# Optimization experiments

Measured on AMD Instinct MI355X. Metric: run time of the kernel, lower is better.

Reference implementation:

```python
import jax, jax.numpy as jnp
import numpy as np

DIM = 768
HEADS = 12
HEAD_DIM = DIM // HEADS
SCALE = HEAD_DIM ** -0.5


def setup_inputs() -> dict:
    key = jax.random.key(0)
    k1, k2, k3, k4, k5 = jax.random.split(key, 5)
    B, N = 4, 2048
    x = jax.random.normal(k1, (B, N, DIM), dtype=jnp.float32)
    # qkv Linear: weight [3*dim, dim], bias [3*dim]
    w_qkv = jax.random.normal(k2, (3 * DIM, DIM), dtype=jnp.float32) * (DIM ** -0.5)
    b_qkv = jax.random.normal(k3, (3 * DIM,), dtype=jnp.float32) * 0.01
    # proj Linear: weight [dim, dim], bias [dim]
    w_proj = jax.random.normal(k4, (DIM, DIM), dtype=jnp.float32) * (DIM ** -0.5)
    b_proj = jax.random.normal(k5, (DIM,), dtype=jnp.float32) * 0.01
    return {"x": x, "w_qkv": w_qkv, "b_qkv": b_qkv, "w_proj": w_proj, "b_proj": b_proj}


def reference(x, w_qkv, b_qkv, w_proj, b_proj):
    B, N, C = x.shape
    qkv = (jnp.einsum('bnc,oc->bno', x, w_qkv) + b_qkv)
    qkv = qkv.reshape(B, N, 3, HEADS, HEAD_DIM).transpose(2, 0, 3, 1, 4)
    q, k, v = qkv[0], qkv[1], qkv[2]
    attn = jnp.einsum('bhqd,bhkd->bhqk', q, k) * SCALE
    attn = jax.nn.softmax(attn, axis=-1)
    out = jnp.einsum('bhqk,bhkd->bhqd', attn, v)  # [B, H, N, Dh]
    out = out.transpose(0, 2, 1, 3).reshape(B, N, C)
    # dropout is identity in eval mode
    return jnp.einsum('bnc,oc->bno', out, w_proj) + b_proj
```

## Files before the change

kernel.cpp:

```cpp
#include <hip/hip_runtime.h>
#include <hip/hip_bf16.h>

using bf16 = __hip_bfloat16;
typedef __bf16 bf16x8 __attribute__((ext_vector_type(8)));
typedef short short4v __attribute__((ext_vector_type(4)));
typedef short short8v __attribute__((ext_vector_type(8)));
typedef float float4v __attribute__((ext_vector_type(4)));

#define DIM   768
#define NH    12
#define HD    64
#define SEQ   2048
#define BATCH 4
#define TOK   (BATCH * SEQ)
#define SCALE_QL2E 0.18033688011112042f

#define NX  (TOK * DIM)
#define NWQ (3 * DIM * DIM)
#define NWP (DIM * DIM)

__device__ __forceinline__ short f2bf(float f) {
  union { bf16 h; short s; } u;
  u.h = __float2bfloat16(f);
  return u.s;
}

union frag8 { short4v h[2]; short8v s; bf16x8 b; };

__device__ __forceinline__ void async_copy16(const bf16* g, short* l) {
  __builtin_amdgcn_global_load_lds(
      (const __attribute__((address_space(1))) unsigned int*)g,
      (__attribute__((address_space(3))) unsigned int*)l, 16, 0, 0);
}

__global__ void __launch_bounds__(256)
cvt3(const float* __restrict__ a, bf16* __restrict__ oa, long na,
     const float* __restrict__ b, bf16* __restrict__ ob, long nb,
     const float* __restrict__ c, bf16* __restrict__ oc, long nc) {
  const long i = ((long)blockIdx.x * 256 + threadIdx.x) * 8;
  const float* src; bf16* dst; long off;
  if (i < na)                { src = a; dst = oa; off = i; }
  else if (i < na + nb)      { src = b; dst = ob; off = i - na; }
  else if (i < na + nb + nc) { src = c; dst = oc; off = i - na - nb; }
  else return;
  const float4v x0 = *(const float4v*)(src + off);
  const float4v x1 = *(const float4v*)(src + off + 4);
  short8v r;
  r[0] = f2bf(x0[0]); r[1] = f2bf(x0[1]); r[2] = f2bf(x0[2]); r[3] = f2bf(x0[3]);
  r[4] = f2bf(x1[0]); r[5] = f2bf(x1[1]); r[6] = f2bf(x1[2]); r[7] = f2bf(x1[3]);
  *(short8v*)(dst + off) = r;
}

__device__ __forceinline__ void gemm_mainloop(const bf16* __restrict__ A,
                                              const bf16* __restrict__ B,
                                              short* As, short* Bs,
                                              float4v acc[4][4]) {
  const int t = threadIdx.x;
  const int w = t >> 6, l = t & 63, lr = l & 15, q = l >> 4;
  const int wr = ((w >> 1) << 6), wc = ((w & 1) << 6);

  const bf16* Ag = A + (t >> 2) * DIM + (t & 3) * 8;
  const bf16* Bg = B + (t >> 2) * DIM + (t & 3) * 8;

  for (int k0 = 0; k0 < DIM; k0 += 32) {
    __syncthreads();
    async_copy16(Ag,            &As[t * 8]);
    async_copy16(Ag + 64 * DIM, &As[2048 + t * 8]);
    async_copy16(Bg,            &Bs[t * 8]);
    async_copy16(Bg + 64 * DIM, &Bs[2048 + t * 8]);
    Ag += 32; Bg += 32;
    __syncthreads();

    bf16x8 af[4], bfv[4];
#pragma unroll
    for (int i = 0; i < 4; ++i)
      af[i] = *(const bf16x8*)&As[(wr + i * 16 + lr) * 32 + q * 8];
#pragma unroll
    for (int j = 0; j < 4; ++j)
      bfv[j] = *(const bf16x8*)&Bs[(wc + j * 16 + lr) * 32 + q * 8];
#pragma unroll
    for (int i = 0; i < 4; ++i)
#pragma unroll
      for (int j = 0; j < 4; ++j)
        acc[i][j] = __builtin_amdgcn_mfma_f32_16x16x32_bf16(af[i], bfv[j],
                                                            acc[i][j], 0, 0, 0);
  }
}

__global__ void __launch_bounds__(256)
gemm_qkv(const bf16* __restrict__ X, const bf16* __restrict__ W,
         const float* __restrict__ bias,
         bf16* __restrict__ qb, bf16* __restrict__ kb, bf16* __restrict__ vb) {
  __shared__ short As[128 * 32];
  __shared__ short Bs[128 * 32];
  const int t = threadIdx.x;
  const int w = t >> 6, l = t & 63, lr = l & 15, q = l >> 4;
  const int wr = ((w >> 1) << 6), wc = ((w & 1) << 6);
  const int row0 = blockIdx.y * 128, col0 = blockIdx.x * 128;

  float4v acc[4][4] = {};
  gemm_mainloop(X + row0 * DIM, W + col0 * DIM, As, Bs, acc);

#pragma unroll
  for (int j = 0; j < 4; ++j) {
    const int gn = col0 + wc + j * 16 + lr;
    const int which = gn / DIM;
    const int cc = gn - which * DIM;
    const int hh = cc >> 6, dd = cc & 63;
    const float bv = bias[gn];
#pragma unroll
    for (int i = 0; i < 4; ++i) {
      const int gm0 = row0 + wr + i * 16 + (q << 2);
      const int b = gm0 >> 11, n0 = gm0 & 2047;
      if (which == 2) {
        short4v pv;
#pragma unroll
        for (int r = 0; r < 4; ++r) pv[r] = f2bf(acc[i][j][r] + bv);
        *(short4v*)&vb[((size_t)(b * NH + hh) * HD + dd) * SEQ + n0] = pv;
      } else {
        bf16* dst = (which == 0) ? qb : kb;
        const float sc = (which == 0) ? SCALE_QL2E : 1.0f;
#pragma unroll
        for (int r = 0; r < 4; ++r)
          dst[((size_t)(b * NH + hh) * SEQ + n0 + r) * HD + dd] =
              __float2bfloat16((acc[i][j][r] + bv) * sc);
      }
    }
  }
}

__global__ void __launch_bounds__(256, 3)
flash_attn(const bf16* __restrict__ Qp, const bf16* __restrict__ Kp,
           const bf16* __restrict__ Vtp, bf16* __restrict__ Op) {
  const int bh = blockIdx.y, qt = blockIdx.x;
  const int t = threadIdx.x, w = t >> 6, l = t & 63, lr = l & 15, q = l >> 4;
  __shared__ short Ks[128 * 72];
  __shared__ short Vt[64 * 136];

  const bf16* Qb = Qp  + (size_t)(bh * SEQ + qt * 128) * HD;
  const bf16* Kb = Kp  + (size_t)bh * SEQ * HD;
  const bf16* Vb = Vtp + (size_t)bh * HD * SEQ;

  const int tr3 = t >> 3, td8 = (t & 7) * 8;
  const int tr4 = t >> 4, tc8 = (t & 15) * 8;

  short8v kr[4], vr[4];
#pragma unroll
  for (int i = 0; i < 4; ++i) {
    kr[i] = *(const short8v*)(Kb + (size_t)(i * 32 + tr3) * HD + td8);
    vr[i] = *(const short8v*)(Vb + (size_t)(i * 16 + tr4) * SEQ + tc8);
  }

#pragma unroll
  for (int i = 0; i < 4; ++i)
    *(short8v*)&Ks[(i * 32 + tr3) * 72 + td8] =
        *(const short8v*)(Qb + (size_t)(i * 32 + tr3) * HD + td8);
  __syncthreads();
  bf16x8 qf[2][2];
#pragma unroll
  for (int it = 0; it < 2; ++it)
#pragma unroll
    for (int kq = 0; kq < 2; ++kq)
      qf[it][kq] = *(const bf16x8*)&Ks[(w * 32 + it * 16 + lr) * 72 + kq * 32 + q * 8];

  float4v o[2][4] = {};
  float l_run[2] = {0.f, 0.f};

  for (int kt = 0; kt < 16; ++kt) {
    __syncthreads();
#pragma unroll
    for (int i = 0; i < 4; ++i) {
      *(short8v*)&Ks[(i * 32 + tr3) * 72 + td8]  = kr[i];
      *(short8v*)&Vt[(i * 16 + tr4) * 136 + tc8] = vr[i];
    }
    __syncthreads();
    if (kt < 15) {
      const int k1 = (kt + 1) * 128;
#pragma unroll
      for (int i = 0; i < 4; ++i) {
        kr[i] = *(const short8v*)(Kb + (size_t)(k1 + i * 32 + tr3) * HD + td8);
        vr[i] = *(const short8v*)(Vb + (size_t)(i * 16 + tr4) * SEQ + k1 + tc8);
      }
    }

    float4v s[8][2] = {};
#pragma unroll
    for (int jn = 0; jn < 8; ++jn) {
      bf16x8 kf[2];
#pragma unroll
      for (int kq = 0; kq < 2; ++kq)
        kf[kq] = *(const bf16x8*)&Ks[(jn * 16 + lr) * 72 + kq * 32 + q * 8];
#pragma unroll
      for (int it = 0; it < 2; ++it)
#pragma unroll
        for (int kq = 0; kq < 2; ++kq)
          s[jn][it] = __builtin_amdgcn_mfma_f32_16x16x32_bf16(kf[kq], qf[it][kq],
                                                              s[jn][it], 0, 0, 0);
    }

    frag8 pf[4][2];
#pragma unroll
    for (int it = 0; it < 2; ++it) {
      float ls = 0.f;
#pragma unroll
      for (int jn = 0; jn < 8; ++jn)
#pragma unroll
        for (int r = 0; r < 4; ++r) {
          const float p = __builtin_amdgcn_exp2f(s[jn][it][r]);
          s[jn][it][r] = p;
          ls += p;
        }
      l_run[it] += ls;
#pragma unroll
      for (int c4 = 0; c4 < 4; ++c4) {
#pragma unroll
        for (int r = 0; r < 4; ++r) {
          pf[c4][it].s[r]     = f2bf(s[2 * c4][it][r]);
          pf[c4][it].s[4 + r] = f2bf(s[2 * c4 + 1][it][r]);
        }
      }
    }

#pragma unroll
    for (int c4 = 0; c4 < 4; ++c4) {
#pragma unroll
      for (int dj = 0; dj < 4; ++dj) {
        frag8 vf;
        vf.h[0] = *(const short4v*)&Vt[(dj * 16 + lr) * 136 + c4 * 32 + (q << 2)];
        vf.h[1] = *(const short4v*)&Vt[(dj * 16 + lr) * 136 + c4 * 32 + 16 + (q << 2)];
#pragma unroll
        for (int it = 0; it < 2; ++it)
          o[it][dj] = __builtin_amdgcn_mfma_f32_16x16x32_bf16(pf[c4][it].b, vf.b,
                                                              o[it][dj], 0, 0, 0);
      }
    }
  }

  const int b = bh / NH, h = bh - b * NH;
#pragma unroll
  for (int it = 0; it < 2; ++it) {
    l_run[it] += __shfl_xor(l_run[it], 16);
    l_run[it] += __shfl_xor(l_run[it], 32);
    const float li = 1.0f / l_run[it];
#pragma unroll
    for (int r = 0; r < 4; ++r) {
      const float linv = __shfl(li, (q << 2) + r, 64);
      const int grow = b * SEQ + qt * 128 + w * 32 + it * 16 + (q << 2) + r;
      bf16* orow = Op + (size_t)grow * DIM + h * HD;
#pragma unroll
      for (int dj = 0; dj < 4; ++dj)
        orow[dj * 16 + lr] = __float2bfloat16(o[it][dj][r] * linv);
    }
  }
}

__global__ void __launch_bounds__(256)
gemm_proj(const bf16* __restrict__ A, const bf16* __restrict__ W,
          const float* __restrict__ bias, float* __restrict__ out) {
  __shared__ short As[128 * 32];
  __shared__ short Bs[128 * 32];
  const int t = threadIdx.x;
  const int w = t >> 6, l = t & 63, lr = l & 15, q = l >> 4;
  const int wr = ((w >> 1) << 6), wc = ((w & 1) << 6);
  const int row0 = blockIdx.y * 128, col0 = blockIdx.x * 128;

  float4v acc[4][4] = {};
  gemm_mainloop(A + row0 * DIM, W + col0 * DIM, As, Bs, acc);

#pragma unroll
  for (int j = 0; j < 4; ++j) {
    const int gn = col0 + wc + j * 16 + lr;
    const float bv = bias[gn];
#pragma unroll
    for (int i = 0; i < 4; ++i) {
#pragma unroll
      for (int r = 0; r < 4; ++r) {
        const int gm = row0 + wr + i * 16 + (q << 2) + r;
        out[(size_t)gm * DIM + gn] = acc[i][j][r] + bv;
      }
    }
  }
}

extern "C" void kernel_launch(void* const* d_in, const int* in_sizes, int n_in,
                              void* d_out, int out_size, void* d_ws, size_t ws_size,
                              hipStream_t stream) {
  const float* x      = (const float*)d_in[0];
  const float* w_qkv  = (const float*)d_in[1];
  const float* b_qkv  = (const float*)d_in[2];
  const float* w_proj = (const float*)d_in[3];
  const float* b_proj = (const float*)d_in[4];
  float* out = (float*)d_out;

  const size_t perbuf = (size_t)BATCH * NH * SEQ * HD;
  bf16* qb  = (bf16*)d_ws;
  bf16* kb  = qb + perbuf;
  bf16* vb  = kb + perbuf;
  bf16* ao  = vb + perbuf;
  bf16* xb  = ao + perbuf;
  bf16* wqb = xb + (size_t)NX;
  bf16* wpb = wqb + (size_t)NWQ;

  const int cvt_blocks = (NX + NWQ + NWP) / 8 / 256;
  cvt3<<<cvt_blocks, 256, 0, stream>>>(x, xb, NX, w_qkv, wqb, NWQ, w_proj, wpb, NWP);
  gemm_qkv <<<dim3(3 * DIM / 128, TOK / 128), 256, 0, stream>>>(xb, wqb, b_qkv, qb, kb, vb);
  flash_attn<<<dim3(SEQ / 128, BATCH * NH),   256, 0, stream>>>(qb, kb, vb, ao);
  gemm_proj <<<dim3(DIM / 128, TOK / 128),    256, 0, stream>>>(ao, wpb, b_proj, out);
}
```

Baseline: 211.9 us.

## Rewrite QKV GEMM as 256x256-tile, 512-thread async double-buffered pipeline

Replaces the 128x128 QKV GEMM with a 256x256 tile kernel using 8 waves. It uses async global-to-LDS copies with double buffering, XOR swizzled LDS layout and interleaved barriers with MFMA priority boosts. It also adds a block-index swizzle for L2 locality. The aim is to hide global load latency and raise MFMA utilisation. The cost is more LDS (128KB) and register pressure, and a fixed launch of 288 blocks that assumes these exact sizes.

Measured after the change: 213.1 us. About the same (+0.6%).

```diff
diff --git a/kernel.cpp b/kernel.cpp
--- a/kernel.cpp
+++ b/kernel.cpp
@@ -87,35 +87,122 @@
   }
 }
 
-__global__ void __launch_bounds__(256)
+#define STG(gp, c, slot, k0)                                                  \
+  async_copy16((gp) + (k0),      &lds[c][slot][t * 8]);                       \
+  async_copy16((gp) + (k0) + 32, &lds[c][slot][4096 + t * 8])
+
+#define RD_A(dst, C, slot)                                                    \
+  _Pragma("unroll") for (int f_ = 0; f_ < 4; ++f_) {                          \
+    dst[f_][0] = *(const bf16x8*)&lds[C][slot][f_ * 1024 + arow32 + acol];    \
+    dst[f_][1] = *(const bf16x8*)&lds[C][slot][4096 + f_ * 1024 + arow32 + acol]; \
+  }
+
+#define RD_B(dst, C, slot)                                                    \
+  _Pragma("unroll") for (int g_ = 0; g_ < 2; ++g_) {                          \
+    dst[g_][0] = *(const bf16x8*)&lds[C][slot][g_ * 2048 + brow32 + acol];    \
+    dst[g_][1] = *(const bf16x8*)&lds[C][slot][4096 + g_ * 2048 + brow32 + acol]; \
+  }
+
+#define MFMA8(AF, BF, MO, NO)                                                 \
+  _Pragma("unroll") for (int f_ = 0; f_ < 4; ++f_)                            \
+  _Pragma("unroll") for (int g_ = 0; g_ < 2; ++g_) {                          \
+    acc[(MO) + f_][(NO) + g_] = __builtin_amdgcn_mfma_f32_16x16x32_bf16(      \
+        AF[f_][0], BF[g_][0], acc[(MO) + f_][(NO) + g_], 0, 0, 0);            \
+    acc[(MO) + f_][(NO) + g_] = __builtin_amdgcn_mfma_f32_16x16x32_bf16(      \
+        AF[f_][1], BF[g_][1], acc[(MO) + f_][(NO) + g_], 0, 0, 0);            \
+  }
+
+#define BARRIER __builtin_amdgcn_s_barrier()
+#define LGKM0 asm volatile("s_waitcnt lgkmcnt(0)" ::: "memory")
+#define VW6 asm volatile("s_waitcnt vmcnt(6)" ::: "memory")
+#define VW0 asm volatile("s_waitcnt vmcnt(0)" ::: "memory")
+#define NOSTG (void)0
+
+#define KTILE(C, ST1, ST2, ST3, ST4, VW)                                      \
+  {                                                                           \
+    bf16x8 a0[4][2], a1[4][2], b0[2][2], b1[2][2];                            \
+    RD_A(a0, C, 0); RD_B(b0, C, 2);                                           \
+    ST1; BARRIER; LGKM0;                                                      \
+    __builtin_amdgcn_s_setprio(1); MFMA8(a0, b0, 0, 0);                       \
+    __builtin_amdgcn_s_setprio(0); BARRIER;                                   \
+    RD_B(b1, C, 3);                                                           \
+    ST2; BARRIER; LGKM0;                                                      \
+    __builtin_amdgcn_s_setprio(1); MFMA8(a0, b1, 0, 2);                       \
+    __builtin_amdgcn_s_setprio(0); BARRIER;                                   \
+    RD_A(a1, C, 1);                                                           \
+    ST3; BARRIER; LGKM0;                                                      \
+    __builtin_amdgcn_s_setprio(1); MFMA8(a1, b0, 4, 0);                       \
+    __builtin_amdgcn_s_setprio(0); BARRIER;                                   \
+    ST4; BARRIER;                                                             \
+    __builtin_amdgcn_s_setprio(1); MFMA8(a1, b1, 4, 2);                       \
+    __builtin_amdgcn_s_setprio(0); VW; BARRIER;                               \
+  }
+
+__global__ void __launch_bounds__(512, 2)
 gemm_qkv(const bf16* __restrict__ X, const bf16* __restrict__ W,
          const float* __restrict__ bias,
          bf16* __restrict__ qb, bf16* __restrict__ kb, bf16* __restrict__ vb) {
-  __shared__ short As[128 * 32];
-  __shared__ short Bs[128 * 32];
+  __shared__ short lds[2][4][8192];
   const int t = threadIdx.x;
   const int w = t >> 6, l = t & 63, lr = l & 15, q = l >> 4;
-  const int wr = ((w >> 1) << 6), wc = ((w & 1) << 6);
-  const int row0 = blockIdx.y * 128, col0 = blockIdx.x * 128;
-
-  float4v acc[4][4] = {};
-  gemm_mainloop(X + row0 * DIM, W + col0 * DIM, As, Bs, acc);
-
-#pragma unroll
-  for (int j = 0; j < 4; ++j) {
-    const int gn = col0 + wc + j * 16 + lr;
+  const int wm = w >> 2, wn = w & 3;
+
+  const int orig = blockIdx.x;
+  const int swz = (orig & 7) * 36 + (orig >> 3);
+  const int tm = swz / 9, tn = swz - tm * 9;
+  const int row0 = tm * 256, col0 = tn * 256;
+
+  const int sr = t >> 2;
+  const int sswz = (((sr >> 3) & 1) << 4) | (((sr >> 1) & 1) << 3);
+  const int scol = (((t & 3) << 3) ^ sswz);
+  const bf16* pa0 = X + (size_t)(row0 +       sr) * DIM + scol;
+  const bf16* pa1 = X + (size_t)(row0 + 128 + sr) * DIM + scol;
+  const bf16* pb0 = W + (size_t)(col0 +       sr) * DIM + scol;
+  const bf16* pb1 = W + (size_t)(col0 + 128 + sr) * DIM + scol;
+
+  const int rswz = (((lr >> 3) & 1) << 4) | (((lr >> 1) & 1) << 3);
+  const int acol = ((q << 3) ^ rswz);
+  const int arow32 = (wm * 16 + lr) * 32;
+  const int brow32 = (wn * 16 + lr) * 32;
+
+  float4v acc[8][4] = {};
+
+  STG(pa0, 0, 0, 0);
+  STG(pb0, 0, 2, 0);
+  STG(pb1, 0, 3, 0);
+  STG(pa1, 0, 1, 0);
+  STG(pa0, 1, 0, 64);
+  STG(pb0, 1, 2, 64);
+  STG(pb1, 1, 3, 64);
+  asm volatile("s_waitcnt vmcnt(6)" ::: "memory");
+  BARRIER;
+
+#pragma unroll 1
+  for (int i = 0; i < 5; ++i) {
+    KTILE(0, STG(pa1, 1, 1, 64),  STG(pa0, 0, 0, 128),
+             STG(pb0, 0, 2, 128), STG(pb1, 0, 3, 128), VW6);
+    KTILE(1, STG(pa1, 0, 1, 128), STG(pa0, 1, 0, 192),
+             STG(pb0, 1, 2, 192), STG(pb1, 1, 3, 192), VW6);
+    pa0 += 128; pa1 += 128; pb0 += 128; pb1 += 128;
+  }
+  KTILE(0, STG(pa1, 1, 1, 64), NOSTG, NOSTG, NOSTG, VW0);
+  KTILE(1, NOSTG, NOSTG, NOSTG, NOSTG, NOSTG);
+
+#pragma unroll
+  for (int nf = 0; nf < 4; ++nf) {
+    const int gn = col0 + nf * 64 + wn * 16 + lr;
     const int which = gn / DIM;
     const int cc = gn - which * DIM;
     const int hh = cc >> 6, dd = cc & 63;
     const float bv = bias[gn];
 #pragma unroll
-    for (int i = 0; i < 4; ++i) {
-      const int gm0 = row0 + wr + i * 16 + (q << 2);
+    for (int mf = 0; mf < 8; ++mf) {
+      const int gm0 = row0 + mf * 32 + wm * 16 + (q << 2);
       const int b = gm0 >> 11, n0 = gm0 & 2047;
       if (which == 2) {
         short4v pv;
 #pragma unroll
-        for (int r = 0; r < 4; ++r) pv[r] = f2bf(acc[i][j][r] + bv);
+        for (int r = 0; r < 4; ++r) pv[r] = f2bf(acc[mf][nf][r] + bv);
         *(short4v*)&vb[((size_t)(b * NH + hh) * HD + dd) * SEQ + n0] = pv;
       } else {
         bf16* dst = (which == 0) ? qb : kb;
@@ -123,7 +210,7 @@
 #pragma unroll
         for (int r = 0; r < 4; ++r)
           dst[((size_t)(b * NH + hh) * SEQ + n0 + r) * HD + dd] =
-              __float2bfloat16((acc[i][j][r] + bv) * sc);
+              __float2bfloat16((acc[mf][nf][r] + bv) * sc);
       }
     }
   }
@@ -303,7 +390,7 @@
 
   const int cvt_blocks = (NX + NWQ + NWP) / 8 / 256;
   cvt3<<<cvt_blocks, 256, 0, stream>>>(x, xb, NX, w_qkv, wqb, NWQ, w_proj, wpb, NWP);
-  gemm_qkv <<<dim3(3 * DIM / 128, TOK / 128), 256, 0, stream>>>(xb, wqb, b_qkv, qb, kb, vb);
-  flash_attn<<<dim3(SEQ / 128, BATCH * NH),   256, 0, stream>>>(qb, kb, vb, ao);
-  gemm_proj <<<dim3(DIM / 128, TOK / 128),    256, 0, stream>>>(ao, wpb, b_proj, out);
-}
+  gemm_qkv <<<dim3(288), 512, 0, stream>>>(xb, wqb, b_qkv, qb, kb, vb);
+  flash_attn<<<dim3(SEQ / 128, BATCH * NH), 256, 0, stream>>>(qb, kb, vb, ao);
+  gemm_proj <<<dim3(DIM / 128, TOK / 128),  256, 0, stream>>>(ao, wpb, b_proj, out);
+}
```
